# Kernel tuning notes

Hardware: AMD Instinct MI355X
Metric: run time of the kernel (lower is better)

The kernel has to match this reference:

```python
import jax, jax.numpy as jnp
import numpy as np

N_NODES = 100000
N_EDGES = 1600000
F_IN = 128
F_HID = 128
F_OUT = 128
N_GRAPHS = 256


def setup_inputs() -> dict:
    key = jax.random.key(0)
    ks = jax.random.split(key, 8)
    x = jax.random.normal(ks[0], (N_NODES, F_IN), dtype=jnp.float32)
    edge_index = jax.random.randint(ks[1], (2, N_EDGES), 0, N_NODES, dtype=jnp.int64)
    batch = jnp.sort(jax.random.randint(ks[2], (N_NODES,), 0, N_GRAPHS, dtype=jnp.int64))
    W1 = jax.random.normal(ks[3], (F_IN, F_HID), dtype=jnp.float32) * 0.05
    b1 = jax.random.normal(ks[4], (F_HID,), dtype=jnp.float32) * 0.05
    W2 = jax.random.normal(ks[5], (F_HID, F_OUT), dtype=jnp.float32) * 0.05
    b2 = jax.random.normal(ks[6], (F_OUT,), dtype=jnp.float32) * 0.05
    return {"x": x, "edge_index": edge_index, "batch": batch,
            "W1": W1, "b1": b1, "W2": W2, "b2": b2}


def reference(x, edge_index, batch, W1, b1, W2, b2):
    n = x.shape[0]
    # --- GCNConv (PyG defaults: add self-loops, symmetric normalization) ---
    loop = jnp.arange(n, dtype=edge_index.dtype)
    row = jnp.concatenate([edge_index[0], loop])  # source nodes
    col = jnp.concatenate([edge_index[1], loop])  # target nodes
    ones = jnp.ones_like(col, dtype=x.dtype)
    deg = jax.ops.segment_sum(ones, col, num_segments=n)          # in-degree incl. self-loop
    dinv = jnp.where(deg > 0, jax.lax.rsqrt(deg), 0.0)
    norm = dinv[row] * dinv[col]                                  # [E+N]
    h = x @ W1                                                    # transform first (PyG order)
    msg = h[row] * norm[:, None]                                  # gather + normalize
    agg = jax.ops.segment_sum(msg, col, num_segments=n) + b1      # scatter-add + bias
    h = jax.nn.relu(agg)
    # --- global_mean_pool over graphs ---
    g_ones = jnp.ones((n,), dtype=x.dtype)
    cnt = jax.ops.segment_sum(g_ones, batch, num_segments=N_GRAPHS)
    pooled = jax.ops.segment_sum(h, batch, num_segments=N_GRAPHS)
    pooled = pooled / jnp.clip(cnt, 1.0)[:, None]
    # --- linear + tanh ---
    return jnp.tanh(pooled @ W2 + b2)
```

## Files before the change

kernel.cpp:

```cpp
#include <hip/hip_runtime.h>
#include <math.h>

#define F 128
#define N_GRAPHS 256
#define BK_SHIFT 8
#define BK_NODES 256
#define BK_CAP 6144
#define BK_SUB 32
#define MAXBK 400
#define NSCAT 512

typedef __attribute__((ext_vector_type(4))) float f32x4;
typedef __attribute__((ext_vector_type(2))) float f32x2;
typedef __attribute__((ext_vector_type(8))) short bf16x8;
typedef __attribute__((ext_vector_type(8))) unsigned short u16x8;

__device__ __forceinline__ unsigned short f2bf(float f) {
    unsigned u = __float_as_uint(f);
    unsigned r = (u + 0x7FFFu + ((u >> 16) & 1u)) >> 16;
    return (unsigned short)r;
}
__device__ __forceinline__ float bf2f(unsigned short u) {
    return __uint_as_float(((unsigned)u) << 16);
}
__device__ __forceinline__ int idxval(const int* raw, int i, bool is32) {
    return is32 ? raw[i] : (int)((const long long*)raw)[i];
}

#if defined(__has_builtin)
#if __has_builtin(__builtin_amdgcn_cvt_pk_f32_fp8) && __has_builtin(__builtin_amdgcn_cvt_pk_fp8_f32)
#define HW_FP8 1
#endif
#endif

__device__ __forceinline__ unsigned char f2fp8(float f) {
#ifdef HW_FP8
    int p = __builtin_amdgcn_cvt_pk_fp8_f32(f, f, 0, false);
    return (unsigned char)(p & 0xFF);
#else
    float a = fabsf(f);
    unsigned s = (f < 0.f) ? 0x80u : 0u;
    if (a >= 448.f) return s | 0x7E;
    if (a < 0.015625f) {
        int m = (int)(a * 512.f + 0.5f);
        return s | (unsigned)m;
    }
    int ex;
    float fr = frexpf(a, &ex);
    int e = ex - 1;
    int q = (int)(a * exp2f((float)(3 - e)) + 0.5f) - 8;
    if (q == 8) { q = 0; e += 1; }
    return s | ((unsigned)(e + 7) << 3) | (unsigned)q;
#endif
}

__device__ __forceinline__ void fp8x16_fma(uint4 v, float w, float* acc) {
#ifdef HW_FP8
    f32x2 p;
    p = __builtin_amdgcn_cvt_pk_f32_fp8((int)v.x, false); acc[0]  += w * p[0]; acc[1]  += w * p[1];
    p = __builtin_amdgcn_cvt_pk_f32_fp8((int)v.x, true);  acc[2]  += w * p[0]; acc[3]  += w * p[1];
    p = __builtin_amdgcn_cvt_pk_f32_fp8((int)v.y, false); acc[4]  += w * p[0]; acc[5]  += w * p[1];
    p = __builtin_amdgcn_cvt_pk_f32_fp8((int)v.y, true);  acc[6]  += w * p[0]; acc[7]  += w * p[1];
    p = __builtin_amdgcn_cvt_pk_f32_fp8((int)v.z, false); acc[8]  += w * p[0]; acc[9]  += w * p[1];
    p = __builtin_amdgcn_cvt_pk_f32_fp8((int)v.z, true);  acc[10] += w * p[0]; acc[11] += w * p[1];
    p = __builtin_amdgcn_cvt_pk_f32_fp8((int)v.w, false); acc[12] += w * p[0]; acc[13] += w * p[1];
    p = __builtin_amdgcn_cvt_pk_f32_fp8((int)v.w, true);  acc[14] += w * p[0]; acc[15] += w * p[1];
#else
    unsigned ww[4] = {v.x, v.y, v.z, v.w};
#pragma unroll
    for (int j = 0; j < 16; ++j) {
        unsigned b = (ww[j >> 2] >> ((j & 3) * 8)) & 0xFF;
        int e = (b >> 3) & 0xF, m = b & 7;
        float val = e ? ldexpf((float)(8 + m), e - 10) : ldexpf((float)m, -9);
        acc[j] += (b & 0x80) ? -(w * val) : (w * val);
    }
#endif
}

__global__ __launch_bounds__(256) void w1t_kernel(
    const float* __restrict__ W1, unsigned short* __restrict__ W1T) {
    int i = blockIdx.x * 256 + threadIdx.x;
    int k = i >> 7, n = i & 127;
    W1T[n * F + k] = f2bf(W1[i]);
}

__global__ __launch_bounds__(256) void scatter_kernel(
    const int* __restrict__ ei_raw, int nE,
    const int* __restrict__ batch_raw, int nN,
    int* __restrict__ cntmat, int* __restrict__ tmp, int nBk) {
    __shared__ int cur[MAXBK];
    __shared__ int cells[MAXBK * BK_SUB];
    int t = threadIdx.x;
    int sb = blockIdx.x;
    bool is32 = (batch_raw[nN - 1] != 0);
    int cs = (nE + NSCAT - 1) / NSCAT;
    int e0 = sb * cs;
    int e1 = min(nE, e0 + cs);

    for (int i = t; i < nBk; i += 256) cur[i] = 0;
    __syncthreads();
    for (int e = e0 + t; e < e1; e += 256) {
        int r = idxval(ei_raw, e, is32);
        int c = idxval(ei_raw, nE + e, is32);
        int b = c >> BK_SHIFT;
        int slot = atomicAdd(&cur[b], 1);
        if (slot < BK_SUB)
            cells[b * BK_SUB + slot] = r | ((c & (BK_NODES - 1)) << 20);
    }
    __syncthreads();
    {
        const int4* src = (const int4*)cells;
        int4* t4 = (int4*)tmp;
        for (int i = t; i < nBk * (BK_SUB / 4); i += 256) {
            int b = i >> 3;
            int w = i & 7;
            t4[((size_t)b * NSCAT + sb) * (BK_SUB / 4) + w] = src[i];
        }
    }
    for (int i = t; i < nBk; i += 256)
        cntmat[i * NSCAT + sb] = min(cur[i], BK_SUB);
}

__global__ __launch_bounds__(256) void gemm_build_kernel(
    const float* __restrict__ x, const unsigned short* __restrict__ W1T,
    const int* __restrict__ tmp, const int* __restrict__ cntmat, int nN,
    unsigned char* __restrict__ h_f8,
    int* __restrict__ off, int* __restrict__ cnt, float* __restrict__ dinv,
    int* __restrict__ csr, int nBk, int nGemm) {
    extern __shared__ char smem[];
    __shared__ int mtot;
    int t = threadIdx.x;

    if (blockIdx.x < (unsigned)nBk) {
        int* ebuf = (int*)smem;
        int* rcnt = ebuf + BK_CAP;
        int* roff = rcnt + NSCAT;
        int* h    = roff + NSCAT;
        int* pfx  = h + BK_NODES;
        int* lcur = pfx + BK_NODES;
        int b = blockIdx.x;
        int nodeLo = b << BK_SHIFT;

        rcnt[t]       = min(cntmat[b * NSCAT + t], BK_SUB);
        rcnt[t + 256] = min(cntmat[b * NSCAT + t + 256], BK_SUB);
        __syncthreads();
        int cA = rcnt[2 * t], cB = rcnt[2 * t + 1];
        int s = cA + cB;
        pfx[t] = s;
        __syncthreads();
        for (int st = 1; st < 256; st <<= 1) {
            int add = (t >= st) ? pfx[t - st] : 0;
            __syncthreads();
            pfx[t] += add;
            __syncthreads();
        }
        if (t == 255) mtot = pfx[255];
        int ex = pfx[t] - s;
        roff[2 * t] = ex;
        roff[2 * t + 1] = ex + cA;
        __syncthreads();
        int m = min(mtot, BK_CAP);

        const int4* t4 = (const int4*)(tmp + (size_t)b * NSCAT * BK_SUB);
        for (int i = t; i < NSCAT * (BK_SUB / 4); i += 256) {
            int sb = i >> 3;
            int k4 = (i & 7) * 4;
            int c = rcnt[sb];
            if (k4 < c) {
                int4 v = t4[i];
                int base0 = roff[sb] + k4;
                int lim = c - k4;
                if (base0 + 0 < BK_CAP && lim > 0) ebuf[base0 + 0] = v.x;
                if (base0 + 1 < BK_CAP && lim > 1) ebuf[base0 + 1] = v.y;
                if (base0 + 2 < BK_CAP && lim > 2) ebuf[base0 + 2] = v.z;
                if (base0 + 3 < BK_CAP && lim > 3) ebuf[base0 + 3] = v.w;
            }
        }
        __syncthreads();

        h[t] = 0;
        __syncthreads();
        for (int i = t; i < m; i += 256)
            atomicAdd(&h[ebuf[i] >> 20], 1);
        __syncthreads();
        int own = h[t];
        int pad = (own + 3) & ~3;
        pfx[t] = pad;
        __syncthreads();
        for (int st = 1; st < 256; st <<= 1) {
            int add = (t >= st) ? pfx[t - st] : 0;
            __syncthreads();
            pfx[t] += add;
            __syncthreads();
        }
        int base = b * BK_CAP;
        int myoff = base + pfx[t] - pad;
        lcur[t] = myoff;
        int node = nodeLo + t;
        if (node < nN) {
            off[node] = myoff;
            cnt[node] = own;
            dinv[node] = rsqrtf((float)(own + 1));
        }
        __syncthreads();
        for (int i = t; i < m; i += 256) {
            int e = ebuf[i];
            int pos = atomicAdd(&lcur[e >> 20], 1);
            csr[pos] = e & 0xFFFFF;
        }
    } else {
        int gb = blockIdx.x - nBk;
        if (gb >= nGemm) return;
        unsigned short* xs = (unsigned short*)smem;
        int row0 = gb * 64;

#pragma unroll
        for (int j = 0; j < 8; ++j) {
            int idx = t + j * 256;
            int rr = idx >> 5, c4 = idx & 31;
            int gr = row0 + rr;
            float4 v = make_float4(0.f, 0.f, 0.f, 0.f);
            if (gr < nN) v = ((const float4*)x)[(size_t)gr * 32 + c4];
            ushort4 o;
            o.x = f2bf(v.x); o.y = f2bf(v.y); o.z = f2bf(v.z); o.w = f2bf(v.w);
            int byte = (rr * 256 + c4 * 8) ^ ((rr & 7) << 4);
            *(ushort4*)((char*)xs + byte) = o;
        }
        __syncthreads();

        int lane = t & 63;
        int w = t >> 6;
        int m0 = (w >> 1) * 32;
        int n0 = (w & 1) * 64;
        int l15 = lane & 15;
        int lg = lane >> 4;

        f32x4 acc[2][4] = {};
#pragma unroll
        for (int ks = 0; ks < 4; ++ks) {
            bf16x8 a[2], b[4];
#pragma unroll
            for (int i = 0; i < 2; ++i) {
                int rr = m0 + i * 16 + l15;
                int byte = (rr * 256 + ks * 64 + lg * 16) ^ ((rr & 7) << 4);
                a[i] = *(const bf16x8*)((const char*)xs + byte);
            }
#pragma unroll
            for (int j = 0; j < 4; ++j) {
                int n = n0 + j * 16 + l15;
                b[j] = *(const bf16x8*)(W1T + (size_t)n * F + ks * 32 + lg * 8);
            }
#pragma unroll
            for (int i = 0; i < 2; ++i)
#pragma unroll
                for (int j = 0; j < 4; ++j)
                    acc[i][j] = __builtin_amdgcn_mfma_f32_16x16x32_bf16(
                        a[i], b[j], acc[i][j], 0, 0, 0);
        }

#pragma unroll
        for (int i = 0; i < 2; ++i) {
#pragma unroll
            for (int rr = 0; rr < 4; ++rr) {
                int gm = row0 + m0 + i * 16 + lg * 4 + rr;
                if (gm < nN) {
#pragma unroll
                    for (int j = 0; j < 4; ++j) {
                        int n = n0 + j * 16 + l15;
                        h_f8[(size_t)gm * F + n] = f2fp8(acc[i][j][rr]);
                    }
                }
            }
        }
    }
}

__global__ __launch_bounds__(256) void aggregate_kernel(
    const unsigned char* __restrict__ h_f8, const int* __restrict__ csr,
    const int* __restrict__ off, const int* __restrict__ cnt,
    const float* __restrict__ dinv, const float* __restrict__ b1,
    unsigned short* __restrict__ agg_bf, int nN) {
    int t = threadIdx.x;
    int lane = t & 7;
    int c = blockIdx.x * 32 + (t >> 3);
    if (c >= nN) return;

    const uint4* h4 = (const uint4*)h_f8;
    int n = cnt[c];
    float dc = rsqrtf((float)(n + 1));
    float acc[16];
#pragma unroll
    for (int j = 0; j < 16; ++j) acc[j] = 0.f;
    fp8x16_fma(h4[(size_t)c * 8 + lane], dc, acc);

    int lo = off[c];
    int k = 0;
    for (; k + 4 <= n; k += 4) {
        int4 e = *(const int4*)(csr + lo + k);
        float w0 = dinv[e.x];
        float w1 = dinv[e.y];
        float w2 = dinv[e.z];
        float w3 = dinv[e.w];
        uint4 v0 = h4[(size_t)e.x * 8 + lane];
        uint4 v1 = h4[(size_t)e.y * 8 + lane];
        uint4 v2 = h4[(size_t)e.z * 8 + lane];
        uint4 v3 = h4[(size_t)e.w * 8 + lane];
        fp8x16_fma(v0, w0, acc);
        fp8x16_fma(v1, w1, acc);
        fp8x16_fma(v2, w2, acc);
        fp8x16_fma(v3, w3, acc);
    }
    if (k < n) {
        int4 e = *(const int4*)(csr + lo + k);
        fp8x16_fma(h4[(size_t)e.x * 8 + lane], dinv[e.x], acc);
        if (k + 1 < n) fp8x16_fma(h4[(size_t)e.y * 8 + lane], dinv[e.y], acc);
        if (k + 2 < n) fp8x16_fma(h4[(size_t)e.z * 8 + lane], dinv[e.z], acc);
    }

    const float* b1p = b1 + lane * 16;
    u16x8 r0, r1;
#pragma unroll
    for (int j = 0; j < 8; ++j) {
        r0[j] = f2bf(fmaxf(b1p[j] + dc * acc[j], 0.f));
        r1[j] = f2bf(fmaxf(b1p[8 + j] + dc * acc[8 + j], 0.f));
    }
    *(u16x8*)(agg_bf + (size_t)c * F + lane * 16) = r0;
    *(u16x8*)(agg_bf + (size_t)c * F + lane * 16 + 8) = r1;
}

__global__ __launch_bounds__(256) void pool_final_kernel(
    const unsigned short* __restrict__ agg_bf,
    const int* __restrict__ batch_raw, int nN,
    const float* __restrict__ W2, const float* __restrict__ b2,
    float* __restrict__ out) {
    int g = blockIdx.x;
    bool is32 = (batch_raw[nN - 1] != 0);
    __shared__ int bounds[2];
    __shared__ float sd[16][F];
    __shared__ float ps[F];
    int t = threadIdx.x;
    if (t < 2) {
        int target = g + t;
        int lo = 0, hi = nN;
        while (lo < hi) {
            int mid = (lo + hi) >> 1;
            if (idxval(batch_raw, mid, is32) < target) lo = mid + 1; else hi = mid;
        }
        bounds[t] = lo;
    }
    __syncthreads();
    int lo = bounds[0], hi = bounds[1];

    int lane = t & 15;
    int grp = t >> 4;
    const u16x8* a8 = (const u16x8*)agg_bf;
    float acc[8];
#pragma unroll
    for (int j = 0; j < 8; ++j) acc[j] = 0.f;
    for (int n = lo + grp; n < hi; n += 16) {
        u16x8 v = a8[(size_t)n * 16 + lane];
#pragma unroll
        for (int j = 0; j < 8; ++j) acc[j] += bf2f(v[j]);
    }
#pragma unroll
    for (int j = 0; j < 8; ++j) sd[grp][lane * 8 + j] = acc[j];
    __syncthreads();

    if (t < F) {
        float s = 0.f;
#pragma unroll
        for (int i = 0; i < 16; ++i) s += sd[i][t];
        float cntf = (float)(hi - lo);
        ps[t] = s / fmaxf(cntf, 1.0f);
    }
    __syncthreads();

    if (t < F) {
        float s = b2[t];
        for (int k = 0; k < F; ++k) s += ps[k] * W2[k * F + t];
        out[g * F + t] = tanhf(s);
    }
}

extern "C" void kernel_launch(void* const* d_in, const int* in_sizes, int n_in,
                              void* d_out, int out_size, void* d_ws, size_t ws_size,
                              hipStream_t stream) {
    const float* x     = (const float*)d_in[0];
    const int*   ei    = (const int*)d_in[1];
    const int*   batch = (const int*)d_in[2];
    const float* W1    = (const float*)d_in[3];
    const float* b1    = (const float*)d_in[4];
    const float* W2    = (const float*)d_in[5];
    const float* b2    = (const float*)d_in[6];
    float* out = (float*)d_out;

    const int nN = in_sizes[2];
    const int nE = in_sizes[1] / 2;
    const int nBk = (nN + BK_NODES - 1) >> BK_SHIFT;
    const int nGemm = (nN + 63) / 64;

    char* ws = (char*)d_ws;
    size_t woff = 0;
    auto take = [&](size_t bytes) {
        void* p = ws + woff;
        woff += (bytes + 15) & ~(size_t)15;
        return p;
    };
    unsigned char*  h_f8   = (unsigned char*)take((size_t)nN * F);
    unsigned short* agg_bf = (unsigned short*)take((size_t)nN * F * 2);
    int*   tmp      = (int*)take((size_t)nBk * NSCAT * BK_SUB * 4);
    int*   csr      = (int*)take((size_t)nBk * BK_CAP * 4);
    int*   cntmat   = (int*)take((size_t)nBk * NSCAT * 4);
    int*   cnt      = (int*)take((size_t)nN * 4);
    int*   off      = (int*)take((size_t)nN * 4);
    float* dinv     = (float*)take((size_t)nN * 4);
    unsigned short* W1T = (unsigned short*)take((size_t)F * F * 2);

    w1t_kernel<<<F * F / 256, 256, 0, stream>>>(W1, W1T);
    scatter_kernel<<<NSCAT, 256, 0, stream>>>(ei, nE, batch, nN, cntmat, tmp, nBk);
    gemm_build_kernel<<<nBk + nGemm, 256, 32768, stream>>>(
        x, W1T, tmp, cntmat, nN, h_f8, off, cnt, dinv, csr, nBk, nGemm);
    aggregate_kernel<<<(nN + 31) / 32, 256, 0, stream>>>(h_f8, csr, off, cnt,
                                                         dinv, b1, agg_bf, nN);
    pool_final_kernel<<<N_GRAPHS, 256, 0, stream>>>(agg_bf, batch, nN, W2, b2, out);
}
```

Before: 115.5 us.

## Degree-sort nodes per bucket to balance aggregate work; skip empty tmp writes

Each bucket block now bitonic-sorts its 256 nodes by in-degree and writes a permutation. The aggregate kernel walks nodes in that order, so the 8-lane groups in a wavefront see similar edge counts and less time is lost to divergence on uneven degrees. The scatter kernel also skips writing unused quads of the per-bucket cell staging. The cost is an extra sort with many barriers in the build kernel, one more indirection per node, and stores to agg_bf that are no longer in node order.

```diff
diff --git a/kernel.cpp b/kernel.cpp
--- a/kernel.cpp
+++ b/kernel.cpp
@@ -114,7 +114,8 @@
         for (int i = t; i < nBk * (BK_SUB / 4); i += 256) {
             int b = i >> 3;
             int w = i & 7;
-            t4[((size_t)b * NSCAT + sb) * (BK_SUB / 4) + w] = src[i];
+            if (w * 4 < cur[b])
+                t4[((size_t)b * NSCAT + sb) * (BK_SUB / 4) + w] = src[i];
         }
     }
     for (int i = t; i < nBk; i += 256)
@@ -126,7 +127,7 @@
     const int* __restrict__ tmp, const int* __restrict__ cntmat, int nN,
     unsigned char* __restrict__ h_f8,
     int* __restrict__ off, int* __restrict__ cnt, float* __restrict__ dinv,
-    int* __restrict__ csr, int nBk, int nGemm) {
+    int* __restrict__ csr, int* __restrict__ perm, int nBk, int nGemm) {
     extern __shared__ char smem[];
     __shared__ int mtot;
     int t = threadIdx.x;
@@ -184,6 +185,26 @@
             atomicAdd(&h[ebuf[i] >> 20], 1);
         __syncthreads();
         int own = h[t];
+        int node = nodeLo + t;
+
+        int* keys = roff;
+        keys[t] = (node < nN) ? ((own << 8) | t) : (0x7FFFFF00 | t);
+        __syncthreads();
+        for (int k = 2; k <= 256; k <<= 1) {
+            for (int j = k >> 1; j > 0; j >>= 1) {
+                int p = t ^ j;
+                int a = keys[t], bb = keys[p];
+                bool up = ((t & k) == 0);
+                int mn = min(a, bb), mx = max(a, bb);
+                __syncthreads();
+                keys[t] = ((t < p) == up) ? mn : mx;
+                __syncthreads();
+            }
+        }
+        int sk = keys[t];
+        perm[b * BK_NODES + t] =
+            ((sk >> 8) == 0x7FFFFF) ? -1 : (nodeLo + (sk & 255));
+
         int pad = (own + 3) & ~3;
         pfx[t] = pad;
         __syncthreads();
@@ -196,7 +217,6 @@
         int base = b * BK_CAP;
         int myoff = base + pfx[t] - pad;
         lcur[t] = myoff;
-        int node = nodeLo + t;
         if (node < nN) {
             off[node] = myoff;
             cnt[node] = own;
@@ -279,11 +299,14 @@
     const unsigned char* __restrict__ h_f8, const int* __restrict__ csr,
     const int* __restrict__ off, const int* __restrict__ cnt,
     const float* __restrict__ dinv, const float* __restrict__ b1,
-    unsigned short* __restrict__ agg_bf, int nN) {
+    const int* __restrict__ perm, unsigned short* __restrict__ agg_bf,
+    int nSlots) {
     int t = threadIdx.x;
     int lane = t & 7;
-    int c = blockIdx.x * 32 + (t >> 3);
-    if (c >= nN) return;
+    int slot = blockIdx.x * 32 + (t >> 3);
+    if (slot >= nSlots) return;
+    int c = perm[slot];
+    if (c < 0) return;
 
     const uint4* h4 = (const uint4*)h_f8;
     int n = cnt[c];
@@ -398,6 +421,7 @@
     const int nE = in_sizes[1] / 2;
     const int nBk = (nN + BK_NODES - 1) >> BK_SHIFT;
     const int nGemm = (nN + 63) / 64;
+    const int nSlots = nBk * BK_NODES;
 
     char* ws = (char*)d_ws;
     size_t woff = 0;
@@ -414,13 +438,14 @@
     int*   cnt      = (int*)take((size_t)nN * 4);
     int*   off      = (int*)take((size_t)nN * 4);
     float* dinv     = (float*)take((size_t)nN * 4);
+    int*   perm     = (int*)take((size_t)nSlots * 4);
     unsigned short* W1T = (unsigned short*)take((size_t)F * F * 2);
 
     w1t_kernel<<<F * F / 256, 256, 0, stream>>>(W1, W1T);
     scatter_kernel<<<NSCAT, 256, 0, stream>>>(ei, nE, batch, nN, cntmat, tmp, nBk);
     gemm_build_kernel<<<nBk + nGemm, 256, 32768, stream>>>(
-        x, W1T, tmp, cntmat, nN, h_f8, off, cnt, dinv, csr, nBk, nGemm);
-    aggregate_kernel<<<(nN + 31) / 32, 256, 0, stream>>>(h_f8, csr, off, cnt,
-                                                         dinv, b1, agg_bf, nN);
+        x, W1T, tmp, cntmat, nN, h_f8, off, cnt, dinv, csr, perm, nBk, nGemm);
+    aggregate_kernel<<<(nSlots + 31) / 32, 256, 0, stream>>>(
+        h_f8, csr, off, cnt, dinv, b1, perm, agg_bf, nSlots);
     pool_final_kernel<<<N_GRAPHS, 256, 0, stream>>>(agg_bf, batch, nN, W2, b2, out);
 }
```

New measurement: 118.2 us. +2.4%, slower.

## Slice fp8 hidden features by column group, fuse W1 transpose, stream CSR build

Applied to the files above, without the earlier changes.

The fp8 hidden matrix is stored in 8 column slices of 16 bytes per node. Each aggregate block now handles a single slice, so the random neighbour gathers touch a working set one eighth the size and should hit cache more often. The W1 transpose moves into the scatter kernel, which removes one launch, and scatter now skips writing empty cells. The CSR build reads tmp twice straight from global memory instead of staging edges in a shared buffer with a prefix scan, which halves shared memory. The cost is eight passes over csr/off/cnt/dinv and narrower 8-byte loads per thread.

```diff
diff --git a/kernel.cpp b/kernel.cpp
--- a/kernel.cpp
+++ b/kernel.cpp
@@ -54,21 +54,17 @@
 #endif
 }
 
-__device__ __forceinline__ void fp8x16_fma(uint4 v, float w, float* acc) {
+__device__ __forceinline__ void fp8x8_fma(uint2 v, float w, float* acc) {
 #ifdef HW_FP8
     f32x2 p;
-    p = __builtin_amdgcn_cvt_pk_f32_fp8((int)v.x, false); acc[0]  += w * p[0]; acc[1]  += w * p[1];
-    p = __builtin_amdgcn_cvt_pk_f32_fp8((int)v.x, true);  acc[2]  += w * p[0]; acc[3]  += w * p[1];
-    p = __builtin_amdgcn_cvt_pk_f32_fp8((int)v.y, false); acc[4]  += w * p[0]; acc[5]  += w * p[1];
-    p = __builtin_amdgcn_cvt_pk_f32_fp8((int)v.y, true);  acc[6]  += w * p[0]; acc[7]  += w * p[1];
-    p = __builtin_amdgcn_cvt_pk_f32_fp8((int)v.z, false); acc[8]  += w * p[0]; acc[9]  += w * p[1];
-    p = __builtin_amdgcn_cvt_pk_f32_fp8((int)v.z, true);  acc[10] += w * p[0]; acc[11] += w * p[1];
-    p = __builtin_amdgcn_cvt_pk_f32_fp8((int)v.w, false); acc[12] += w * p[0]; acc[13] += w * p[1];
-    p = __builtin_amdgcn_cvt_pk_f32_fp8((int)v.w, true);  acc[14] += w * p[0]; acc[15] += w * p[1];
+    p = __builtin_amdgcn_cvt_pk_f32_fp8((int)v.x, false); acc[0] += w * p[0]; acc[1] += w * p[1];
+    p = __builtin_amdgcn_cvt_pk_f32_fp8((int)v.x, true);  acc[2] += w * p[0]; acc[3] += w * p[1];
+    p = __builtin_amdgcn_cvt_pk_f32_fp8((int)v.y, false); acc[4] += w * p[0]; acc[5] += w * p[1];
+    p = __builtin_amdgcn_cvt_pk_f32_fp8((int)v.y, true);  acc[6] += w * p[0]; acc[7] += w * p[1];
 #else
-    unsigned ww[4] = {v.x, v.y, v.z, v.w};
-#pragma unroll
-    for (int j = 0; j < 16; ++j) {
+    unsigned ww[2] = {v.x, v.y};
+#pragma unroll
+    for (int j = 0; j < 8; ++j) {
         unsigned b = (ww[j >> 2] >> ((j & 3) * 8)) & 0xFF;
         int e = (b >> 3) & 0xF, m = b & 7;
         float val = e ? ldexpf((float)(8 + m), e - 10) : ldexpf((float)m, -9);
@@ -77,21 +73,20 @@
 #endif
 }
 
-__global__ __launch_bounds__(256) void w1t_kernel(
-    const float* __restrict__ W1, unsigned short* __restrict__ W1T) {
-    int i = blockIdx.x * 256 + threadIdx.x;
-    int k = i >> 7, n = i & 127;
-    W1T[n * F + k] = f2bf(W1[i]);
-}
-
 __global__ __launch_bounds__(256) void scatter_kernel(
     const int* __restrict__ ei_raw, int nE,
     const int* __restrict__ batch_raw, int nN,
+    const float* __restrict__ W1, unsigned short* __restrict__ W1T,
     int* __restrict__ cntmat, int* __restrict__ tmp, int nBk) {
     __shared__ int cur[MAXBK];
     __shared__ int cells[MAXBK * BK_SUB];
     int t = threadIdx.x;
     int sb = blockIdx.x;
+    if (sb < 64) {
+        int i = sb * 256 + t;
+        int k = i >> 7, n = i & 127;
+        W1T[n * F + k] = f2bf(W1[i]);
+    }
     bool is32 = (batch_raw[nN - 1] != 0);
     int cs = (nE + NSCAT - 1) / NSCAT;
     int e0 = sb * cs;
@@ -114,7 +109,8 @@
         for (int i = t; i < nBk * (BK_SUB / 4); i += 256) {
             int b = i >> 3;
             int w = i & 7;
-            t4[((size_t)b * NSCAT + sb) * (BK_SUB / 4) + w] = src[i];
+            if (w * 4 < cur[b])
+                t4[((size_t)b * NSCAT + sb) * (BK_SUB / 4) + w] = src[i];
         }
     }
     for (int i = t; i < nBk; i += 256)
@@ -124,18 +120,15 @@
 __global__ __launch_bounds__(256) void gemm_build_kernel(
     const float* __restrict__ x, const unsigned short* __restrict__ W1T,
     const int* __restrict__ tmp, const int* __restrict__ cntmat, int nN,
-    unsigned char* __restrict__ h_f8,
+    unsigned char* __restrict__ h_sl,
     int* __restrict__ off, int* __restrict__ cnt, float* __restrict__ dinv,
     int* __restrict__ csr, int nBk, int nGemm) {
     extern __shared__ char smem[];
-    __shared__ int mtot;
     int t = threadIdx.x;
 
     if (blockIdx.x < (unsigned)nBk) {
-        int* ebuf = (int*)smem;
-        int* rcnt = ebuf + BK_CAP;
-        int* roff = rcnt + NSCAT;
-        int* h    = roff + NSCAT;
+        int* rcnt = (int*)smem;
+        int* h    = rcnt + NSCAT;
         int* pfx  = h + BK_NODES;
         int* lcur = pfx + BK_NODES;
         int b = blockIdx.x;
@@ -143,23 +136,8 @@
 
         rcnt[t]       = min(cntmat[b * NSCAT + t], BK_SUB);
         rcnt[t + 256] = min(cntmat[b * NSCAT + t + 256], BK_SUB);
+        h[t] = 0;
         __syncthreads();
-        int cA = rcnt[2 * t], cB = rcnt[2 * t + 1];
-        int s = cA + cB;
-        pfx[t] = s;
-        __syncthreads();
-        for (int st = 1; st < 256; st <<= 1) {
-            int add = (t >= st) ? pfx[t - st] : 0;
-            __syncthreads();
-            pfx[t] += add;
-            __syncthreads();
-        }
-        if (t == 255) mtot = pfx[255];
-        int ex = pfx[t] - s;
-        roff[2 * t] = ex;
-        roff[2 * t + 1] = ex + cA;
-        __syncthreads();
-        int m = min(mtot, BK_CAP);
 
         const int4* t4 = (const int4*)(tmp + (size_t)b * NSCAT * BK_SUB);
         for (int i = t; i < NSCAT * (BK_SUB / 4); i += 256) {
@@ -168,21 +146,15 @@
             int c = rcnt[sb];
             if (k4 < c) {
                 int4 v = t4[i];
-                int base0 = roff[sb] + k4;
                 int lim = c - k4;
-                if (base0 + 0 < BK_CAP && lim > 0) ebuf[base0 + 0] = v.x;
-                if (base0 + 1 < BK_CAP && lim > 1) ebuf[base0 + 1] = v.y;
-                if (base0 + 2 < BK_CAP && lim > 2) ebuf[base0 + 2] = v.z;
-                if (base0 + 3 < BK_CAP && lim > 3) ebuf[base0 + 3] = v.w;
+                atomicAdd(&h[v.x >> 20], 1);
+                if (lim > 1) atomicAdd(&h[v.y >> 20], 1);
+                if (lim > 2) atomicAdd(&h[v.z >> 20], 1);
+                if (lim > 3) atomicAdd(&h[v.w >> 20], 1);
             }
         }
         __syncthreads();
 
-        h[t] = 0;
-        __syncthreads();
-        for (int i = t; i < m; i += 256)
-            atomicAdd(&h[ebuf[i] >> 20], 1);
-        __syncthreads();
         int own = h[t];
         int pad = (own + 3) & ~3;
         pfx[t] = pad;
@@ -193,8 +165,7 @@
             pfx[t] += add;
             __syncthreads();
         }
-        int base = b * BK_CAP;
-        int myoff = base + pfx[t] - pad;
+        int myoff = b * BK_CAP + pfx[t] - pad;
         lcur[t] = myoff;
         int node = nodeLo + t;
         if (node < nN) {
@@ -203,10 +174,31 @@
             dinv[node] = rsqrtf((float)(own + 1));
         }
         __syncthreads();
-        for (int i = t; i < m; i += 256) {
-            int e = ebuf[i];
-            int pos = atomicAdd(&lcur[e >> 20], 1);
-            csr[pos] = e & 0xFFFFF;
+
+        for (int i = t; i < NSCAT * (BK_SUB / 4); i += 256) {
+            int sb = i >> 3;
+            int k4 = (i & 7) * 4;
+            int c = rcnt[sb];
+            if (k4 < c) {
+                int4 v = t4[i];
+                int lim = c - k4;
+                {
+                    int pos = atomicAdd(&lcur[v.x >> 20], 1);
+                    csr[pos] = v.x & 0xFFFFF;
+                }
+                if (lim > 1) {
+                    int pos = atomicAdd(&lcur[v.y >> 20], 1);
+                    csr[pos] = v.y & 0xFFFFF;
+                }
+                if (lim > 2) {
+                    int pos = atomicAdd(&lcur[v.z >> 20], 1);
+                    csr[pos] = v.z & 0xFFFFF;
+                }
+                if (lim > 3) {
+                    int pos = atomicAdd(&lcur[v.w >> 20], 1);
+                    csr[pos] = v.w & 0xFFFFF;
+                }
+            }
         }
     } else {
         int gb = blockIdx.x - nBk;
@@ -258,6 +250,7 @@
                         a[i], b[j], acc[i][j], 0, 0, 0);
         }
 
+        int s0 = n0 >> 4;
 #pragma unroll
         for (int i = 0; i < 2; ++i) {
 #pragma unroll
@@ -266,8 +259,8 @@
                 if (gm < nN) {
 #pragma unroll
                     for (int j = 0; j < 4; ++j) {
-                        int n = n0 + j * 16 + l15;
-                        h_f8[(size_t)gm * F + n] = f2fp8(acc[i][j][rr]);
+                        size_t byte = (((size_t)(s0 + j) * nN + gm) << 4) + l15;
+                        h_sl[byte] = f2fp8(acc[i][j][rr]);
                     }
                 }
             }
@@ -276,56 +269,59 @@
 }
 
 __global__ __launch_bounds__(256) void aggregate_kernel(
-    const unsigned char* __restrict__ h_f8, const int* __restrict__ csr,
+    const unsigned char* __restrict__ h_sl, const int* __restrict__ csr,
     const int* __restrict__ off, const int* __restrict__ cnt,
     const float* __restrict__ dinv, const float* __restrict__ b1,
     unsigned short* __restrict__ agg_bf, int nN) {
     int t = threadIdx.x;
-    int lane = t & 7;
-    int c = blockIdx.x * 32 + (t >> 3);
+    int s = blockIdx.x & 7;
+    int c = (blockIdx.x >> 3) * 128 + (t >> 1);
     if (c >= nN) return;
-
-    const uint4* h4 = (const uint4*)h_f8;
+    int half = t & 1;
+
+    const uint2* h2 = (const uint2*)h_sl;
+    size_t sbase = (size_t)s * nN;
     int n = cnt[c];
     float dc = rsqrtf((float)(n + 1));
-    float acc[16];
-#pragma unroll
-    for (int j = 0; j < 16; ++j) acc[j] = 0.f;
-    fp8x16_fma(h4[(size_t)c * 8 + lane], dc, acc);
+    float acc[8];
+#pragma unroll
+    for (int j = 0; j < 8; ++j) acc[j] = 0.f;
+    fp8x8_fma(h2[(sbase + c) * 2 + half], dc, acc);
 
     int lo = off[c];
     int k = 0;
     for (; k + 4 <= n; k += 4) {
         int4 e = *(const int4*)(csr + lo + k);
-        float w0 = dinv[e.x];
-        float w1 = dinv[e.y];
-        float w2 = dinv[e.z];
-        float w3 = dinv[e.w];
-        uint4 v0 = h4[(size_t)e.x * 8 + lane];
-        uint4 v1 = h4[(size_t)e.y * 8 + lane];
-        uint4 v2 = h4[(size_t)e.z * 8 + lane];
-        uint4 v3 = h4[(size_t)e.w * 8 + lane];
-        fp8x16_fma(v0, w0, acc);
-        fp8x16_fma(v1, w1, acc);
-        fp8x16_fma(v2, w2, acc);
-        fp8x16_fma(v3, w3, acc);
+        float w0 = dinv[e.x], w1 = dinv[e.y], w2 = dinv[e.z], w3 = dinv[e.w];
+        uint2 v0 = h2[(sbase + e.x) * 2 + half];
+        uint2 v1 = h2[(sbase + e.y) * 2 + half];
+        uint2 v2 = h2[(sbase + e.z) * 2 + half];
+        uint2 v3 = h2[(sbase + e.w) * 2 + half];
+        fp8x8_fma(v0, w0, acc);
+        fp8x8_fma(v1, w1, acc);
+        fp8x8_fma(v2, w2, acc);
+        fp8x8_fma(v3, w3, acc);
     }
     if (k < n) {
         int4 e = *(const int4*)(csr + lo + k);
-        fp8x16_fma(h4[(size_t)e.x * 8 + lane], dinv[e.x], acc);
-        if (k + 1 < n) fp8x16_fma(h4[(size_t)e.y * 8 + lane], dinv[e.y], acc);
-        if (k + 2 < n) fp8x16_fma(h4[(size_t)e.z * 8 + lane], dinv[e.z], acc);
-    }
-
-    const float* b1p = b1 + lane * 16;
-    u16x8 r0, r1;
-#pragma unroll
-    for (int j = 0; j < 8; ++j) {
-        r0[j] = f2bf(fmaxf(b1p[j] + dc * acc[j], 0.f));
-        r1[j] = f2bf(fmaxf(b1p[8 + j] + dc * acc[8 + j], 0.f));
-    }
-    *(u16x8*)(agg_bf + (size_t)c * F + lane * 16) = r0;
-    *(u16x8*)(agg_bf + (size_t)c * F + lane * 16 + 8) = r1;
+        fp8x8_fma(h2[(sbase + e.x) * 2 + half], dinv[e.x], acc);
+        if (k + 1 < n) fp8x8_fma(h2[(sbase + e.y) * 2 + half], dinv[e.y], acc);
+        if (k + 2 < n) fp8x8_fma(h2[(sbase + e.z) * 2 + half], dinv[e.z], acc);
+    }
+
+    const float* b1p = b1 + s * 16 + half * 8;
+    ushort4 r0, r1;
+    r0.x = f2bf(fmaxf(b1p[0] + dc * acc[0], 0.f));
+    r0.y = f2bf(fmaxf(b1p[1] + dc * acc[1], 0.f));
+    r0.z = f2bf(fmaxf(b1p[2] + dc * acc[2], 0.f));
+    r0.w = f2bf(fmaxf(b1p[3] + dc * acc[3], 0.f));
+    r1.x = f2bf(fmaxf(b1p[4] + dc * acc[4], 0.f));
+    r1.y = f2bf(fmaxf(b1p[5] + dc * acc[5], 0.f));
+    r1.z = f2bf(fmaxf(b1p[6] + dc * acc[6], 0.f));
+    r1.w = f2bf(fmaxf(b1p[7] + dc * acc[7], 0.f));
+    unsigned short* dst = agg_bf + (size_t)c * F + s * 16 + half * 8;
+    *(ushort4*)dst = r0;
+    *(ushort4*)(dst + 4) = r1;
 }
 
 __global__ __launch_bounds__(256) void pool_final_kernel(
@@ -406,7 +402,7 @@
         woff += (bytes + 15) & ~(size_t)15;
         return p;
     };
-    unsigned char*  h_f8   = (unsigned char*)take((size_t)nN * F);
+    unsigned char*  h_sl   = (unsigned char*)take((size_t)nN * F);
     unsigned short* agg_bf = (unsigned short*)take((size_t)nN * F * 2);
     int*   tmp      = (int*)take((size_t)nBk * NSCAT * BK_SUB * 4);
     int*   csr      = (int*)take((size_t)nBk * BK_CAP * 4);
@@ -416,11 +412,11 @@
     float* dinv     = (float*)take((size_t)nN * 4);
     unsigned short* W1T = (unsigned short*)take((size_t)F * F * 2);
 
-    w1t_kernel<<<F * F / 256, 256, 0, stream>>>(W1, W1T);
-    scatter_kernel<<<NSCAT, 256, 0, stream>>>(ei, nE, batch, nN, cntmat, tmp, nBk);
-    gemm_build_kernel<<<nBk + nGemm, 256, 32768, stream>>>(
-        x, W1T, tmp, cntmat, nN, h_f8, off, cnt, dinv, csr, nBk, nGemm);
-    aggregate_kernel<<<(nN + 31) / 32, 256, 0, stream>>>(h_f8, csr, off, cnt,
-                                                         dinv, b1, agg_bf, nN);
+    scatter_kernel<<<NSCAT, 256, 0, stream>>>(ei, nE, batch, nN, W1, W1T,
+                                              cntmat, tmp, nBk);
+    gemm_build_kernel<<<nBk + nGemm, 256, 16384, stream>>>(
+        x, W1T, tmp, cntmat, nN, h_sl, off, cnt, dinv, csr, nBk, nGemm);
+    aggregate_kernel<<<8 * ((nN + 127) / 128), 256, 0, stream>>>(
+        h_sl, csr, off, cnt, dinv, b1, agg_bf, nN);
     pool_final_kernel<<<N_GRAPHS, 256, 0, stream>>>(agg_bf, batch, nN, W2, b2, out);
 }
```

Result: slower. 184.9 us (+60.1%).
